# Optimization experiments

Measured on AMD Instinct MI355X. Metric: run time of the kernel, lower is better.

Reference implementation:

```python
import jax, jax.numpy as jnp
import numpy as np

D_VOCAB, D_MODEL, N_CTX, D_MLP, D_HEAD, N_HEADS, N_LAYERS = 32000, 1024, 2048, 4096, 64, 16, 4
BATCH, SEQ = 2, 2048


def setup_inputs() -> dict:
    key = jax.random.key(0)
    ks = jax.random.split(key, 12)
    sd = 1.0 / np.sqrt(D_MODEL)
    inp = {
        'tokens': jax.random.randint(ks[0], (BATCH, SEQ), 0, D_VOCAB),
        'W_E': jax.random.normal(ks[1], (D_MODEL, D_VOCAB), jnp.float32) * sd,
        'W_pos': jax.random.normal(ks[2], (N_CTX, D_MODEL), jnp.float32) * sd,
        'W_K': jax.random.normal(ks[3], (N_LAYERS, N_HEADS, D_HEAD, D_MODEL), jnp.float32) * sd,
        'W_Q': jax.random.normal(ks[4], (N_LAYERS, N_HEADS, D_HEAD, D_MODEL), jnp.float32) * sd,
        'W_V': jax.random.normal(ks[5], (N_LAYERS, N_HEADS, D_HEAD, D_MODEL), jnp.float32) * sd,
        'W_O': jax.random.normal(ks[6], (N_LAYERS, D_MODEL, D_HEAD * N_HEADS), jnp.float32) * sd,
        'W_in': jax.random.normal(ks[7], (N_LAYERS, D_MLP, D_MODEL), jnp.float32) * sd,
        'b_in': jnp.zeros((N_LAYERS, D_MLP), jnp.float32),
        'W_out': jax.random.normal(ks[8], (N_LAYERS, D_MODEL, D_MLP), jnp.float32) * sd,
        'b_out': jnp.zeros((N_LAYERS, D_MODEL), jnp.float32),
        'W_U': jax.random.normal(ks[9], (D_MODEL, D_VOCAB), jnp.float32) / np.sqrt(D_VOCAB),
    }
    return inp


def reference(tokens, W_E, W_pos, W_K, W_Q, W_V, W_O, W_in, b_in, W_out, b_out, W_U):
    P = tokens.shape[-1]
    # Embed: einsum('dbp->bpd', W_E[:, x])  ==  W_E.T[tokens]
    x = W_E.T[tokens]                      # [b, p, d]
    x = x + W_pos[:P]                      # PosEmbed
    causal = jnp.tril(jnp.ones((P, P), dtype=bool))  # mask[q, p]: p <= q
    scale = 1.0 / np.sqrt(D_HEAD)
    for l in range(N_LAYERS):
        # --- Attention ---
        k = jnp.einsum('ihd,bpd->biph', W_K[l], x)
        q = jnp.einsum('ihd,bpd->biph', W_Q[l], x)
        v = jnp.einsum('ihd,bpd->biph', W_V[l], x)
        scores = jnp.einsum('biph,biqh->biqp', k, q)
        # tril(scores) - 1e10*(1-mask)  ==  where(mask, scores, -1e10)
        masked = jnp.where(causal, scores, jnp.float32(-1e10))
        attn = jax.nn.softmax(masked * scale, axis=-1)   # softmax over keys p
        z = jnp.einsum('biph,biqp->biqh', v, attn)       # [b, i, q, h]
        z_flat = jnp.transpose(z, (0, 2, 1, 3)).reshape(z.shape[0], P, -1)  # b q (i h)
        attn_out = jnp.einsum('df,bqf->bqd', W_O[l], z_flat)
        x = x + attn_out
        # --- MLP (ReLU) ---
        pre = jnp.einsum('md,bpd->bpm', W_in[l], x) + b_in[l]
        post = jax.nn.relu(pre)
        x = x + jnp.einsum('dm,bpm->bpd', W_out[l], post) + b_out[l]
    return x @ W_U                          # logits [b, p, d_vocab]
```

## Files before the change

### kernel.cpp

```cpp
#include <hip/hip_runtime.h>
#include <hip/hip_bf16.h>
#include <math.h>

#define DV   32000
#define DM   1024
#define DMLP 4096
#define DH   64
#define NH   16
#define NL   4
#define BATCH 2
#define S    2048
#define MTOK (BATCH*S)

typedef __bf16 bf16_t;
typedef bf16_t bf16x8 __attribute__((ext_vector_type(8)));
typedef float  f32x4  __attribute__((ext_vector_type(4)));

#define AS1 __attribute__((address_space(1)))
#define AS3 __attribute__((address_space(3)))

__device__ __forceinline__ void gload16(const bf16_t* g, bf16_t* l) {
    __builtin_amdgcn_global_load_lds((const AS1 void*)g, (AS3 void*)l, 16, 0, 0);
}

__device__ __forceinline__ unsigned short bfbits(float v) {
    union { bf16_t b; unsigned short u; } c; c.b = (bf16_t)v; return c.u;
}

template<int MODE, bool BIAS, bool RELU>
__global__ __launch_bounds__(512, 1)
void gemm256(const bf16_t* __restrict__ A, const bf16_t* __restrict__ Bm,
             char* __restrict__ Out, int ldc,
             const float* __restrict__ bias, int K)
{
    const int mb = blockIdx.x, nb = blockIdx.y;

    __shared__ alignas(16) bf16_t lds[2][2][2][128*64];

    const int tid  = threadIdx.x;
    const int wave = tid >> 6, lane = tid & 63;
    const int wm = wave >> 2, wn = wave & 3;
    const int l16 = lane & 15, lh = lane >> 4;

    const bf16_t* Abase = A  + (long)(mb*256)*K;
    const bf16_t* Bbase = Bm + (long)(nb*256)*K;

    const int c0 = tid,      r0 = c0 >> 3, lc0 = (c0 & 7) ^ (r0 & 7);
    const int c1 = 512 + tid,r1 = c1 >> 3, lc1 = (c1 & 7) ^ (r1 & 7);

    auto stage = [&](int buf, int mat, int half, int k0) {
        const bf16_t* src = (mat ? Bbase : Abase) + (long)(half*128)*K + k0;
        bf16_t* dst = &lds[buf][mat][half][0];
        gload16(&src[(long)r0*K + lc0*8], dst + c0*8);
        gload16(&src[(long)r1*K + lc1*8], dst + c1*8);
    };

    f32x4 acc[8][4];
#pragma unroll
    for (int i=0;i<8;i++)
#pragma unroll
        for (int j=0;j<4;j++) { f32x4 zv={0.f,0.f,0.f,0.f}; acc[i][j]=zv; }

    const int NT = K >> 6;
    stage(0,0,0,0); stage(0,0,1,0); stage(0,1,0,0); stage(0,1,1,0);

    int cur = 0;
    for (int kt = 0; kt < NT; ++kt) {
        const int nxt = cur ^ 1;
        const int k1 = (kt+1) << 6;
        const bool more = (kt+1 < NT);

        if (more) {
            stage(nxt,0,0,k1);
            asm volatile("s_waitcnt vmcnt(2)" ::: "memory");
        } else {
            asm volatile("s_waitcnt vmcnt(0)" ::: "memory");
        }
        asm volatile("s_barrier" ::: "memory");

        bf16x8 af[4][2], bfr[4][2];
#pragma unroll
        for (int i=0;i<4;i++) {
            int ra = i*16 + l16;
#pragma unroll
            for (int kk=0;kk<2;kk++)
                af[i][kk] = *(const bf16x8*)&lds[cur][0][wm][ra*64 + (((kk*4+lh)^(ra&7))*8)];
        }
#pragma unroll
        for (int j=0;j<2;j++) {
            int rb = (wn&1)*64 + j*16 + l16;
#pragma unroll
            for (int kk=0;kk<2;kk++)
                bfr[j][kk] = *(const bf16x8*)&lds[cur][1][wn>>1][rb*64 + (((kk*4+lh)^(rb&7))*8)];
        }
        __builtin_amdgcn_s_setprio(1);
#pragma unroll
        for (int kk=0;kk<2;kk++)
#pragma unroll
            for (int i=0;i<4;i++)
#pragma unroll
                for (int j=0;j<2;j++)
                    acc[i][j] = __builtin_amdgcn_mfma_f32_16x16x32_bf16(af[i][kk], bfr[j][kk], acc[i][j], 0,0,0);
        __builtin_amdgcn_s_setprio(0);

        if (more) stage(nxt,0,1,k1);
#pragma unroll
        for (int j=2;j<4;j++) {
            int rb = (wn&1)*64 + j*16 + l16;
#pragma unroll
            for (int kk=0;kk<2;kk++)
                bfr[j][kk] = *(const bf16x8*)&lds[cur][1][wn>>1][rb*64 + (((kk*4+lh)^(rb&7))*8)];
        }
        __builtin_amdgcn_s_setprio(1);
#pragma unroll
        for (int kk=0;kk<2;kk++)
#pragma unroll
            for (int i=0;i<4;i++)
#pragma unroll
                for (int j=2;j<4;j++)
                    acc[i][j] = __builtin_amdgcn_mfma_f32_16x16x32_bf16(af[i][kk], bfr[j][kk], acc[i][j], 0,0,0);
        __builtin_amdgcn_s_setprio(0);

        if (more) stage(nxt,1,0,k1);
#pragma unroll
        for (int i=0;i<4;i++) {
            int ra = (i+4)*16 + l16;
#pragma unroll
            for (int kk=0;kk<2;kk++)
                af[i][kk] = *(const bf16x8*)&lds[cur][0][wm][ra*64 + (((kk*4+lh)^(ra&7))*8)];
        }
        __builtin_amdgcn_s_setprio(1);
#pragma unroll
        for (int kk=0;kk<2;kk++)
#pragma unroll
            for (int i=0;i<4;i++)
#pragma unroll
                for (int j=0;j<2;j++)
                    acc[i+4][j] = __builtin_amdgcn_mfma_f32_16x16x32_bf16(af[i][kk], bfr[j][kk], acc[i+4][j], 0,0,0);
        __builtin_amdgcn_s_setprio(0);

        if (more) stage(nxt,1,1,k1);
        __builtin_amdgcn_s_setprio(1);
#pragma unroll
        for (int kk=0;kk<2;kk++)
#pragma unroll
            for (int i=0;i<4;i++)
#pragma unroll
                for (int j=2;j<4;j++)
                    acc[i+4][j] = __builtin_amdgcn_mfma_f32_16x16x32_bf16(af[i][kk], bfr[j][kk], acc[i+4][j], 0,0,0);
        __builtin_amdgcn_s_setprio(0);

        asm volatile("s_barrier" ::: "memory");
        cur = nxt;
    }

#pragma unroll
    for (int i=0;i<8;i++) {
        int row0 = mb*256 + wm*128 + i*16 + lh*4;
#pragma unroll
        for (int j=0;j<4;j++) {
            int col = nb*256 + wn*64 + j*16 + l16;
            float bv = BIAS ? bias[col] : 0.0f;
#pragma unroll
            for (int r=0;r<4;r++) {
                int row = row0 + r;
                float v = acc[i][j][r] + bv;
                if (RELU) v = v > 0.f ? v : 0.f;
                if constexpr (MODE == 0)
                    ((bf16_t*)Out)[(long)row*ldc + col] = (bf16_t)v;
                else
                    ((float*)Out)[(long)row*ldc + col] = v;
            }
        }
    }
}

template<int BM, int BN, int MODE, bool BIAS, bool RELU>
__global__ __launch_bounds__(256)
void gemm_tn(const bf16_t* __restrict__ A, long sA,
             const bf16_t* __restrict__ Bm, long sB,
             char* __restrict__ Out, long sC, int ldc,
             const float* __restrict__ bias,
             float* __restrict__ resid, bf16_t* __restrict__ residb,
             int K)
{
    constexpr int BK = 64;
    constexpr int WM = BM/2, WN = BN/2;
    constexpr int FM = WM/16, FN = WN/16;
    constexpr int APASS = (BM*BK)/(256*8);
    constexpr int BPASS = (BN*BK)/(256*8);

    const int mb = blockIdx.x, nb = blockIdx.y;

    __shared__ alignas(16) bf16_t As[BM*BK];
    __shared__ alignas(16) bf16_t Bs[BN*BK];

    const int tid  = threadIdx.x;
    const int wave = tid >> 6, lane = tid & 63;
    const int wm = wave >> 1, wn = wave & 1;
    const int l16 = lane & 15, lh = lane >> 4;
    const long z = blockIdx.z;

    const bf16_t* Ab = A  + z*sA + (long)mb*BM*K;
    const bf16_t* Bb = Bm + z*sB + (long)nb*BN*K;

    f32x4 acc[FM][FN];
#pragma unroll
    for (int i=0;i<FM;i++)
#pragma unroll
        for (int j=0;j<FN;j++) { f32x4 zv = {0.f,0.f,0.f,0.f}; acc[i][j] = zv; }

    for (int k0 = 0; k0 < K; k0 += BK) {
        __syncthreads();
#pragma unroll
        for (int u=0; u<APASS; ++u) {
            int c = u*256 + tid;
            int row = c >> 3, lc = (c & 7) ^ (row & 7);
            gload16(&Ab[(long)row*K + k0 + lc*8], &As[c*8]);
        }
#pragma unroll
        for (int u=0; u<BPASS; ++u) {
            int c = u*256 + tid;
            int row = c >> 3, lc = (c & 7) ^ (row & 7);
            gload16(&Bb[(long)row*K + k0 + lc*8], &Bs[c*8]);
        }
        __syncthreads();

        bf16x8 af[FM][2], bfr[FN][2];
#pragma unroll
        for (int kk=0;kk<2;kk++) {
#pragma unroll
            for (int i=0;i<FM;i++) {
                int row = wm*WM + i*16 + l16;
                int pw = (kk*4 + lh) ^ (row & 7);
                af[i][kk] = *(const bf16x8*)&As[row*BK + pw*8];
            }
#pragma unroll
            for (int j=0;j<FN;j++) {
                int row = wn*WN + j*16 + l16;
                int pw = (kk*4 + lh) ^ (row & 7);
                bfr[j][kk] = *(const bf16x8*)&Bs[row*BK + pw*8];
            }
        }
#pragma unroll
        for (int kk=0;kk<2;kk++)
#pragma unroll
            for (int i=0;i<FM;i++)
#pragma unroll
                for (int j=0;j<FN;j++)
                    acc[i][j] = __builtin_amdgcn_mfma_f32_16x16x32_bf16(af[i][kk], bfr[j][kk], acc[i][j], 0,0,0);
    }

#pragma unroll
    for (int i=0;i<FM;i++) {
        int row0 = mb*BM + wm*WM + i*16 + lh*4;
#pragma unroll
        for (int j=0;j<FN;j++) {
            int col = nb*BN + wn*WN + j*16 + l16;
            float bv = BIAS ? bias[col] : 0.0f;
#pragma unroll
            for (int r=0;r<4;r++) {
                int row = row0 + r;
                float v = acc[i][j][r] + bv;
                if (RELU) v = v > 0.f ? v : 0.f;
                if constexpr (MODE == 0) {
                    long off = z*sC + (long)row*ldc + col;
                    ((bf16_t*)Out)[off] = (bf16_t)v;
                } else if constexpr (MODE == 1) {
                    long off = z*sC + (long)row*ldc + col;
                    ((float*)Out)[off] = v;
                } else {
                    long o2 = (long)row*ldc + col;
                    float nv = resid[o2] + v;
                    resid[o2]  = nv;
                    residb[o2] = (bf16_t)nv;
                }
            }
        }
    }
}

__global__ __launch_bounds__(256)
void flash_attn(const bf16_t* __restrict__ qkvf,
                const bf16_t* __restrict__ vtg,
                bf16_t* __restrict__ zf)
{
    const int qt = blockIdx.x;
    const int bh = blockIdx.y;
    const int b  = bh >> 4, hd = bh & 15;

    __shared__ alignas(16) bf16_t Kl[64*64];
    __shared__ alignas(16) bf16_t Vtl[64*64];
    __shared__ alignas(16) bf16_t Pl[4*32*64];

    const int tid = threadIdx.x;
    const int wave = tid >> 6, lane = tid & 63;
    const int l16 = lane & 15, lh = lane >> 4;
    const int wq_lo = qt*128 + wave*32;
    bf16_t* Pw = Pl + wave*32*64;

    bf16x8 qr[2][2];
#pragma unroll
    for (int qf=0; qf<2; qf++) {
        int qg = wq_lo + qf*16 + l16;
#pragma unroll
        for (int dhh=0; dhh<2; dhh++)
            qr[qf][dhh] = *(const bf16x8*)&qkvf[((long)b*S + qg)*3072 + hd*64 + dhh*32 + lh*8];
    }

    f32x4 o[4][2];
#pragma unroll
    for (int d=0; d<4; d++)
#pragma unroll
        for (int qf=0; qf<2; qf++) { f32x4 zv={0.f,0.f,0.f,0.f}; o[d][qf]=zv; }
    float mrun[2] = {-1e30f, -1e30f};
    float lrun[2] = {0.f, 0.f};

    const int nt = 2*(qt+1);
    const float C = 0.125f;

    for (int t = 0; t < nt; ++t) {
        const int kv0 = t*64;
        __syncthreads();
#pragma unroll
        for (int u=0; u<2; ++u) {
            int c = u*256 + tid;
            int row = c >> 3, lc = (c & 7) ^ (row & 7);
            gload16(&qkvf[((long)b*S + kv0 + row)*3072 + 1024 + hd*64 + lc*8], &Kl[c*8]);
        }
#pragma unroll
        for (int u=0; u<2; ++u) {
            int c = u*256 + tid;
            int row = c >> 3, lc = (c & 7) ^ (row & 7);
            gload16(&vtg[((long)bh*DH + row)*S + kv0 + lc*8], &Vtl[c*8]);
        }
        __syncthreads();

        f32x4 s[4][2];
#pragma unroll
        for (int f=0; f<4; f++)
#pragma unroll
            for (int qf=0; qf<2; qf++) { f32x4 zv={0.f,0.f,0.f,0.f}; s[f][qf]=zv; }
        __builtin_amdgcn_s_setprio(1);
#pragma unroll
        for (int f=0; f<4; f++) {
            int krow = f*16 + l16;
#pragma unroll
            for (int dhh=0; dhh<2; dhh++) {
                bf16x8 kfr = *(const bf16x8*)&Kl[krow*64 + (((dhh*4+lh) ^ (krow&7))*8)];
#pragma unroll
                for (int qf=0; qf<2; qf++)
                    s[f][qf] = __builtin_amdgcn_mfma_f32_16x16x32_bf16(kfr, qr[qf][dhh], s[f][qf], 0,0,0);
            }
        }
        __builtin_amdgcn_s_setprio(0);

        const bool needmask = (kv0 + 64 > wq_lo);

#pragma unroll
        for (int qf=0; qf<2; qf++) {
            int qg = wq_lo + qf*16 + l16;
            float pmax = -1e30f;
#pragma unroll
            for (int f=0; f<4; f++)
#pragma unroll
                for (int r=0; r<4; r++) {
                    float sv = s[f][qf][r];
                    if (needmask && (kv0 + f*16 + lh*4 + r > qg)) { sv = -1e30f; s[f][qf][r] = sv; }
                    pmax = fmaxf(pmax, sv);
                }
            pmax = fmaxf(pmax, __shfl_xor(pmax, 16));
            pmax = fmaxf(pmax, __shfl_xor(pmax, 32));
            float mnew = fmaxf(mrun[qf], pmax);
            float corr = __expf((mrun[qf] - mnew)*C);
            mrun[qf] = mnew;
            lrun[qf] *= corr;
#pragma unroll
            for (int d=0; d<4; d++) o[d][qf] *= corr;
            float lsum = 0.f;
            int qloc = qf*16 + l16;
#pragma unroll
            for (int f=0; f<4; f++) {
                ushort4 pk;
                float p0 = __expf((s[f][qf][0]-mnew)*C);
                float p1 = __expf((s[f][qf][1]-mnew)*C);
                float p2 = __expf((s[f][qf][2]-mnew)*C);
                float p3 = __expf((s[f][qf][3]-mnew)*C);
                lsum += (p0+p1) + (p2+p3);
                pk.x = bfbits(p0); pk.y = bfbits(p1); pk.z = bfbits(p2); pk.w = bfbits(p3);
                int phys = (f*2 + (lh>>1)) ^ (qloc & 7);
                *(ushort4*)&Pw[qloc*64 + phys*8 + (lh&1)*4] = pk;
            }
            lrun[qf] += lsum;
        }

#pragma unroll
        for (int kh=0; kh<2; kh++) {
            bf16x8 pb[2];
#pragma unroll
            for (int qf=0; qf<2; qf++) {
                int qloc = qf*16 + l16;
                pb[qf] = *(const bf16x8*)&Pw[qloc*64 + (((kh*4+lh) ^ (qloc&7))*8)];
            }
            __builtin_amdgcn_s_setprio(1);
#pragma unroll
            for (int d=0; d<4; d++) {
                int vrow = d*16 + l16;
                bf16x8 va = *(const bf16x8*)&Vtl[vrow*64 + (((kh*4+lh) ^ (vrow&7))*8)];
#pragma unroll
                for (int qf=0; qf<2; qf++)
                    o[d][qf] = __builtin_amdgcn_mfma_f32_16x16x32_bf16(va, pb[qf], o[d][qf], 0,0,0);
            }
            __builtin_amdgcn_s_setprio(0);
        }
    }

#pragma unroll
    for (int qf=0; qf<2; qf++) {
        float lt = lrun[qf];
        lt += __shfl_xor(lt, 16);
        lt += __shfl_xor(lt, 32);
        float inv = 1.0f / lt;
        int qg = wq_lo + qf*16 + l16;
#pragma unroll
        for (int d=0; d<4; d++) {
            ushort4 ov;
            ov.x = bfbits(o[d][qf][0]*inv);
            ov.y = bfbits(o[d][qf][1]*inv);
            ov.z = bfbits(o[d][qf][2]*inv);
            ov.w = bfbits(o[d][qf][3]*inv);
            *(ushort4*)&zf[((long)b*S + qg)*DM + hd*64 + d*16 + lh*4] = ov;
        }
    }
}

__global__ __launch_bounds__(256) void k_conv_qkv(
    const float* __restrict__ Wq, const float* __restrict__ Wk,
    const float* __restrict__ Wv, bf16_t* __restrict__ out)
{
    long idx = (long)blockIdx.x*256 + threadIdx.x;
    long l = idx / (3072L*DM);
    long r = idx % (3072L*DM);
    int row = (int)(r / DM), d = (int)(r % DM);
    int sel = row >> 10, rr = row & 1023;
    const float* src = sel==0 ? Wq : (sel==1 ? Wk : Wv);
    out[idx] = (bf16_t)src[(l*1024 + rr)*(long)DM + d];
}

__global__ __launch_bounds__(256) void k_conv(const float* __restrict__ src,
                                              bf16_t* __restrict__ dst, long n)
{
    long i = ((long)blockIdx.x*256 + threadIdx.x)*4;
    if (i >= n) return;
    float4 v = *(const float4*)&src[i];
    dst[i+0]=(bf16_t)v.x; dst[i+1]=(bf16_t)v.y; dst[i+2]=(bf16_t)v.z; dst[i+3]=(bf16_t)v.w;
}

__global__ __launch_bounds__(256) void k_trans_wu(const float* __restrict__ W,
                                                  bf16_t* __restrict__ out)
{
    __shared__ float tile[32][33];
    int n0 = blockIdx.x*32, k0 = blockIdx.y*32;
    int tx = threadIdx.x & 31, ty = threadIdx.x >> 5;
#pragma unroll
    for (int u=0;u<4;u++)
        tile[ty+u*8][tx] = W[(long)(k0+ty+u*8)*DV + n0+tx];
    __syncthreads();
#pragma unroll
    for (int u=0;u<4;u++)
        out[(long)(n0+ty+u*8)*DM + k0+tx] = (bf16_t)tile[tx][ty+u*8];
}

__global__ __launch_bounds__(256) void k_embed(const int* __restrict__ tok,
    const float* __restrict__ WE, const float* __restrict__ Wpos,
    float* __restrict__ xf, bf16_t* __restrict__ xb)
{
    int bp = blockIdx.x;
    int p  = bp & (S-1);
    int t  = tok[bp];
#pragma unroll
    for (int u=0;u<4;u++) {
        int d = u*256 + threadIdx.x;
        float v = WE[(long)d*DV + t] + Wpos[(long)p*DM + d];
        xf[(long)bp*DM + d] = v;
        xb[(long)bp*DM + d] = (bf16_t)v;
    }
}

__global__ __launch_bounds__(256) void k_permute_v(const bf16_t* __restrict__ qkv,
    bf16_t* __restrict__ vt)
{
    long idx = (long)blockIdx.x*256 + threadIdx.x;
    long bp = idx >> 10; int m = (int)(idx & 1023);
    int b = (int)(bp >> 11), p = (int)(bp & 2047);
    int i = m >> 6, hh = m & 63;
    vt[(((long)b*NH + i)*DH + hh)*S + p] = qkv[bp*3072 + 2048 + m];
}

extern "C" void kernel_launch(void* const* d_in, const int* in_sizes, int n_in,
                              void* d_out, int out_size, void* d_ws, size_t ws_size,
                              hipStream_t stream)
{
    const int*   tokens = (const int*)d_in[0];
    const float* W_E    = (const float*)d_in[1];
    const float* W_pos  = (const float*)d_in[2];
    const float* W_K    = (const float*)d_in[3];
    const float* W_Q    = (const float*)d_in[4];
    const float* W_V    = (const float*)d_in[5];
    const float* W_O    = (const float*)d_in[6];
    const float* W_in   = (const float*)d_in[7];
    const float* b_in   = (const float*)d_in[8];
    const float* W_out  = (const float*)d_in[9];
    const float* b_out  = (const float*)d_in[10];
    const float* W_U    = (const float*)d_in[11];
    float* out = (float*)d_out;

    char* ws = (char*)d_ws;
    long off = 0;
    auto alloc = [&](long bytes)->char* {
        char* p = ws + off; off += (bytes + 255) & ~255L; return p;
    };
    bf16_t* wqkv = (bf16_t*)alloc((long)NL*3072*DM*2);
    bf16_t* wo   = (bf16_t*)alloc((long)NL*DM*DM*2);
    bf16_t* win  = (bf16_t*)alloc((long)NL*DMLP*DM*2);
    bf16_t* wout = (bf16_t*)alloc((long)NL*DM*DMLP*2);
    bf16_t* wut  = (bf16_t*)alloc((long)DV*DM*2);
    float*  xf   = (float*)alloc((long)MTOK*DM*4);
    bf16_t* xb   = (bf16_t*)alloc((long)MTOK*DM*2);
    bf16_t* qkvf = (bf16_t*)alloc((long)MTOK*3072*2);
    bf16_t* vt   = (bf16_t*)alloc((long)BATCH*NH*S*DH*2);
    bf16_t* zf   = (bf16_t*)alloc((long)MTOK*DM*2);
    bf16_t* post = (bf16_t*)alloc((long)MTOK*DMLP*2);

    k_conv_qkv<<<(int)(((long)NL*3072*DM)/256), 256, 0, stream>>>(W_Q, W_K, W_V, wqkv);
    k_conv<<<(int)(((long)NL*DM*DM)/1024),   256, 0, stream>>>(W_O,   wo,   (long)NL*DM*DM);
    k_conv<<<(int)(((long)NL*DMLP*DM)/1024), 256, 0, stream>>>(W_in,  win,  (long)NL*DMLP*DM);
    k_conv<<<(int)(((long)NL*DM*DMLP)/1024), 256, 0, stream>>>(W_out, wout, (long)NL*DM*DMLP);
    k_trans_wu<<<dim3(DV/32, DM/32), 256, 0, stream>>>(W_U, wut);

    k_embed<<<MTOK, 256, 0, stream>>>(tokens, W_E, W_pos, xf, xb);

    for (int l = 0; l < NL; ++l) {
        gemm256<0,false,false><<<dim3(MTOK/256, 3072/256), 512, 0, stream>>>(
            xb, wqkv + (long)l*3072*DM, (char*)qkvf, 3072, nullptr, DM);
        k_permute_v<<<(int)(((long)MTOK*1024)/256), 256, 0, stream>>>(qkvf, vt);

        flash_attn<<<dim3(S/128, BATCH*NH), 256, 0, stream>>>(qkvf, vt, zf);

        gemm_tn<64,128,2,false,false><<<dim3(MTOK/64, DM/128, 1), 256, 0, stream>>>(
            zf, 0L, wo + (long)l*DM*DM, 0L, nullptr, 0L, DM,
            nullptr, xf, xb, DM);
        gemm256<0,true,true><<<dim3(MTOK/256, DMLP/256), 512, 0, stream>>>(
            xb, win + (long)l*DMLP*DM, (char*)post, DMLP,
            b_in + (long)l*DMLP, DM);
        gemm_tn<64,128,2,true,false><<<dim3(MTOK/64, DM/128, 1), 256, 0, stream>>>(
            post, 0L, wout + (long)l*DM*DMLP, 0L, nullptr, 0L, DM,
            b_out + (long)l*DM, xf, xb, DMLP);
    }

    gemm256<1,false,false><<<dim3(MTOK/256, DV/256), 512, 0, stream>>>(
        xb, wut, (char*)out, DV, nullptr, DM);
}
```

Before: 1.670 ms.

## Tile V permute, pre-transpose W_E, enlarge residual GEMM tiles, nontemporal logits

Replaces the scalar V permute with an LDS-tiled transpose so reads and writes are coalesced. W_E is transposed into bf16 once so the embedding gather reads contiguous rows, at the cost of an extra full-vocab transpose and bf16 rounding of embeddings. The output-projection and MLP-down GEMMs move to 128x128 tiles. Logit stores become nontemporal to avoid polluting cache.

```diff
diff --git a/kernel.cpp b/kernel.cpp
--- a/kernel.cpp
+++ b/kernel.cpp
@@ -26,6 +26,9 @@
 __device__ __forceinline__ unsigned short bfbits(float v) {
     union { bf16_t b; unsigned short u; } c; c.b = (bf16_t)v; return c.u;
 }
+__device__ __forceinline__ float b2f(unsigned short u) {
+    union { float f; unsigned v; } c; c.v = ((unsigned)u) << 16; return c.f;
+}
 
 template<int MODE, bool BIAS, bool RELU>
 __global__ __launch_bounds__(512, 1)
@@ -45,8 +48,8 @@
     const bf16_t* Abase = A  + (long)(mb*256)*K;
     const bf16_t* Bbase = Bm + (long)(nb*256)*K;
 
-    const int c0 = tid,      r0 = c0 >> 3, lc0 = (c0 & 7) ^ (r0 & 7);
-    const int c1 = 512 + tid,r1 = c1 >> 3, lc1 = (c1 & 7) ^ (r1 & 7);
+    const int c0 = tid,       r0 = c0 >> 3, lc0 = (c0 & 7) ^ (r0 & 7);
+    const int c1 = 512 + tid, r1 = c1 >> 3, lc1 = (c1 & 7) ^ (r1 & 7);
 
     auto stage = [&](int buf, int mat, int half, int k0) {
         const bf16_t* src = (mat ? Bbase : Abase) + (long)(half*128)*K + k0;
@@ -169,7 +172,7 @@
                 if constexpr (MODE == 0)
                     ((bf16_t*)Out)[(long)row*ldc + col] = (bf16_t)v;
                 else
-                    ((float*)Out)[(long)row*ldc + col] = v;
+                    __builtin_nontemporal_store(v, &((float*)Out)[(long)row*ldc + col]);
             }
         }
     }
@@ -456,15 +459,15 @@
     dst[i+0]=(bf16_t)v.x; dst[i+1]=(bf16_t)v.y; dst[i+2]=(bf16_t)v.z; dst[i+3]=(bf16_t)v.w;
 }
 
-__global__ __launch_bounds__(256) void k_trans_wu(const float* __restrict__ W,
-                                                  bf16_t* __restrict__ out)
+__global__ __launch_bounds__(256) void k_trans(const float* __restrict__ W,
+                                               bf16_t* __restrict__ out, int NC)
 {
     __shared__ float tile[32][33];
     int n0 = blockIdx.x*32, k0 = blockIdx.y*32;
     int tx = threadIdx.x & 31, ty = threadIdx.x >> 5;
 #pragma unroll
     for (int u=0;u<4;u++)
-        tile[ty+u*8][tx] = W[(long)(k0+ty+u*8)*DV + n0+tx];
+        tile[ty+u*8][tx] = W[(long)(k0+ty+u*8)*NC + n0+tx];
     __syncthreads();
 #pragma unroll
     for (int u=0;u<4;u++)
@@ -472,29 +475,42 @@
 }
 
 __global__ __launch_bounds__(256) void k_embed(const int* __restrict__ tok,
-    const float* __restrict__ WE, const float* __restrict__ Wpos,
+    const bf16_t* __restrict__ WEt, const float* __restrict__ Wpos,
     float* __restrict__ xf, bf16_t* __restrict__ xb)
 {
     int bp = blockIdx.x;
     int p  = bp & (S-1);
     int t  = tok[bp];
-#pragma unroll
-    for (int u=0;u<4;u++) {
-        int d = u*256 + threadIdx.x;
-        float v = WE[(long)d*DV + t] + Wpos[(long)p*DM + d];
-        xf[(long)bp*DM + d] = v;
-        xb[(long)bp*DM + d] = (bf16_t)v;
-    }
-}
-
-__global__ __launch_bounds__(256) void k_permute_v(const bf16_t* __restrict__ qkv,
+    int d  = threadIdx.x*4;
+    ushort4 e = *(const ushort4*)&WEt[(long)t*DM + d];
+    float4  w = *(const float4*)&Wpos[(long)p*DM + d];
+    float4 v;
+    v.x = b2f(e.x)+w.x; v.y = b2f(e.y)+w.y; v.z = b2f(e.z)+w.z; v.w = b2f(e.w)+w.w;
+    *(float4*)&xf[(long)bp*DM + d] = v;
+    ushort4 o;
+    o.x = bfbits(v.x); o.y = bfbits(v.y); o.z = bfbits(v.z); o.w = bfbits(v.w);
+    *(ushort4*)&xb[(long)bp*DM + d] = o;
+}
+
+__global__ __launch_bounds__(256) void k_permv(const bf16_t* __restrict__ qkv,
     bf16_t* __restrict__ vt)
 {
-    long idx = (long)blockIdx.x*256 + threadIdx.x;
-    long bp = idx >> 10; int m = (int)(idx & 1023);
-    int b = (int)(bp >> 11), p = (int)(bp & 2047);
-    int i = m >> 6, hh = m & 63;
-    vt[(((long)b*NH + i)*DH + hh)*S + p] = qkv[bp*3072 + 2048 + m];
+    __shared__ bf16_t tile[64][66];
+    const int p0 = blockIdx.x*64;
+    const int bh = blockIdx.y;
+    const int b  = bh >> 4, hd = bh & 15;
+    const int tx = threadIdx.x & 63, ty = threadIdx.x >> 6;
+#pragma unroll
+    for (int u=0;u<16;u++) {
+        int r = u*4 + ty;
+        tile[r][tx] = qkv[((long)b*S + p0 + r)*3072 + 2048 + hd*64 + tx];
+    }
+    __syncthreads();
+#pragma unroll
+    for (int u=0;u<16;u++) {
+        int hh = u*4 + ty;
+        vt[(((long)bh)*DH + hh)*S + p0 + tx] = tile[tx][hh];
+    }
 }
 
 extern "C" void kernel_launch(void* const* d_in, const int* in_sizes, int n_in,
@@ -525,6 +541,7 @@
     bf16_t* win  = (bf16_t*)alloc((long)NL*DMLP*DM*2);
     bf16_t* wout = (bf16_t*)alloc((long)NL*DM*DMLP*2);
     bf16_t* wut  = (bf16_t*)alloc((long)DV*DM*2);
+    bf16_t* wet  = (bf16_t*)alloc((long)DV*DM*2);
     float*  xf   = (float*)alloc((long)MTOK*DM*4);
     bf16_t* xb   = (bf16_t*)alloc((long)MTOK*DM*2);
     bf16_t* qkvf = (bf16_t*)alloc((long)MTOK*3072*2);
@@ -536,24 +553,25 @@
     k_conv<<<(int)(((long)NL*DM*DM)/1024),   256, 0, stream>>>(W_O,   wo,   (long)NL*DM*DM);
     k_conv<<<(int)(((long)NL*DMLP*DM)/1024), 256, 0, stream>>>(W_in,  win,  (long)NL*DMLP*DM);
     k_conv<<<(int)(((long)NL*DM*DMLP)/1024), 256, 0, stream>>>(W_out, wout, (long)NL*DM*DMLP);
-    k_trans_wu<<<dim3(DV/32, DM/32), 256, 0, stream>>>(W_U, wut);
-
-    k_embed<<<MTOK, 256, 0, stream>>>(tokens, W_E, W_pos, xf, xb);
+    k_trans<<<dim3(DV/32, DM/32), 256, 0, stream>>>(W_U, wut, DV);
+    k_trans<<<dim3(DV/32, DM/32), 256, 0, stream>>>(W_E, wet, DV);
+
+    k_embed<<<MTOK, 256, 0, stream>>>(tokens, wet, W_pos, xf, xb);
 
     for (int l = 0; l < NL; ++l) {
         gemm256<0,false,false><<<dim3(MTOK/256, 3072/256), 512, 0, stream>>>(
             xb, wqkv + (long)l*3072*DM, (char*)qkvf, 3072, nullptr, DM);
-        k_permute_v<<<(int)(((long)MTOK*1024)/256), 256, 0, stream>>>(qkvf, vt);
+        k_permv<<<dim3(S/64, BATCH*NH), 256, 0, stream>>>(qkvf, vt);
 
         flash_attn<<<dim3(S/128, BATCH*NH), 256, 0, stream>>>(qkvf, vt, zf);
 
-        gemm_tn<64,128,2,false,false><<<dim3(MTOK/64, DM/128, 1), 256, 0, stream>>>(
+        gemm_tn<128,128,2,false,false><<<dim3(MTOK/128, DM/128, 1), 256, 0, stream>>>(
             zf, 0L, wo + (long)l*DM*DM, 0L, nullptr, 0L, DM,
             nullptr, xf, xb, DM);
         gemm256<0,true,true><<<dim3(MTOK/256, DMLP/256), 512, 0, stream>>>(
             xb, win + (long)l*DMLP*DM, (char*)post, DMLP,
             b_in + (long)l*DMLP, DM);
-        gemm_tn<64,128,2,true,false><<<dim3(MTOK/64, DM/128, 1), 256, 0, stream>>>(
+        gemm_tn<128,128,2,true,false><<<dim3(MTOK/128, DM/128, 1), 256, 0, stream>>>(
             post, 0L, wout + (long)l*DM*DMLP, 0L, nullptr, 0L, DM,
             b_out + (long)l*DM, xf, xb, DMLP);
     }
```

Result: no change. 1.697 ms (+1.6%).
